# Kernel optimization log

Measured on AMD Instinct MI355X. Metric: run time of the kernel, lower is better.

## Reference

```python
import jax, jax.numpy as jnp
import numpy as np

N_HEAD = 16
N_KV_HEADS = 4
N_REP = 4
HEAD_DIM = 128
N_EMBD = 2048
EPS = 1e-5
ROPE_BASE = 10000.0


def setup_inputs() -> dict:
    key = jax.random.key(0)
    ks = jax.random.split(key, 5)
    B, T, C = 2, 2048, N_EMBD
    s = 0.02
    return {
        "x": jax.random.normal(ks[0], (B, T, C), dtype=jnp.float32),
        "wq": jax.random.normal(ks[1], (C, N_HEAD * HEAD_DIM), dtype=jnp.float32) * s,
        "wk": jax.random.normal(ks[2], (C, N_KV_HEADS * HEAD_DIM), dtype=jnp.float32) * s,
        "wv": jax.random.normal(ks[3], (C, N_KV_HEADS * HEAD_DIM), dtype=jnp.float32) * s,
        "wc": jax.random.normal(ks[4], (C, C), dtype=jnp.float32) * s,
        "q_norm_w": jnp.ones((HEAD_DIM,), dtype=jnp.float32),
        "k_norm_w": jnp.ones((HEAD_DIM,), dtype=jnp.float32),
    }


def _rmsnorm(x, w):
    # norm in fp32, scale by weight (matches RMSNorm.forward)
    xf = x.astype(jnp.float32)
    rms = jax.lax.rsqrt(jnp.mean(xf * xf, axis=-1, keepdims=True) + EPS)
    return (xf * rms).astype(x.dtype) * w


def _rope(x, cos, sin):
    # x: [B,T,H,D]; cos/sin: [T, D//2]; interleaved even/odd rotation
    xf = x.astype(jnp.float32)
    xe = xf[..., 0::2]
    xo = xf[..., 1::2]
    c = cos[None, :, None, :]
    s = sin[None, :, None, :]
    ye = xe * c - xo * s
    yo = xe * s + xo * c
    y = jnp.stack((ye, yo), axis=-1).reshape(x.shape)
    return y.astype(x.dtype)


def reference(x, wq, wk, wv, wc, q_norm_w, k_norm_w):
    B, T, C = x.shape
    q = (x @ wq).reshape(B, T, N_HEAD, HEAD_DIM)
    k = (x @ wk).reshape(B, T, N_KV_HEADS, HEAD_DIM)
    v = (x @ wv).reshape(B, T, N_KV_HEADS, HEAD_DIM)

    q = _rmsnorm(q, q_norm_w)
    k = _rmsnorm(k, k_norm_w)

    inv_freq = 1.0 / (ROPE_BASE ** (jnp.arange(0, HEAD_DIM, 2, dtype=jnp.float32) / HEAD_DIM))
    theta = jnp.arange(T, dtype=jnp.float32)[:, None] * inv_freq[None, :]  # [T, D//2]
    cos, sin = jnp.cos(theta), jnp.sin(theta)
    q = _rope(q, cos, sin)
    k = _rope(k, cos, sin)

    # GQA: repeat kv heads (repeat_kv with n_rep)
    k = jnp.repeat(k, N_REP, axis=2)  # [B,T,H,D]
    v = jnp.repeat(v, N_REP, axis=2)

    scale = 1.0 / jnp.sqrt(jnp.float32(HEAD_DIM))
    scores = jnp.einsum("bthd,bshd->bhts", q, k) * scale  # [B,H,T,S]
    causal = jnp.tril(jnp.ones((T, T), dtype=bool))
    scores = jnp.where(causal[None, None], scores, jnp.finfo(scores.dtype).min)
    attn = jax.nn.softmax(scores, axis=-1)
    y = jnp.einsum("bhts,bshd->bthd", attn, v).reshape(B, T, C)
    return y @ wc
```

## Files before the change

kernel.cpp:

```cpp
#include <hip/hip_runtime.h>
#include <hip/hip_bf16.h>
#include <cstdint>
#include <cstddef>

using bf16 = __hip_bfloat16;
typedef __attribute__((ext_vector_type(8))) short short8;
typedef __attribute__((ext_vector_type(4))) float f32x4;
typedef __attribute__((ext_vector_type(16))) float f32x16;

#define T_SEQ 2048
#define NHEAD 16
#define NKV 4
#define HD 128
#define CE 2048

__device__ __forceinline__ void gl_lds16(const void* g, void* l) {
  __builtin_amdgcn_global_load_lds(
      (const __attribute__((address_space(1))) unsigned int*)g,
      (__attribute__((address_space(3))) unsigned int*)l, 16, 0, 0);
}

__device__ __forceinline__ unsigned int cvtpk_bf16(float lo, float hi) {
  unsigned int r;
  asm("v_cvt_pk_bf16_f32 %0, %1, %2" : "=v"(r) : "v"(lo), "v"(hi));
  return r;
}

__device__ __forceinline__ void plswap(unsigned int& x, unsigned int& y, int hi) {
#if __has_builtin(__builtin_amdgcn_permlane32_swap)
  auto r = __builtin_amdgcn_permlane32_swap(x, y, false, false);
  x = r[0];
  y = r[1];
#else
  unsigned int xp = (unsigned int)__shfl_xor((int)x, 32);
  unsigned int yp = (unsigned int)__shfl_xor((int)y, 32);
  unsigned int nx = hi ? yp : x;
  unsigned int ny = hi ? y : xp;
  x = nx;
  y = ny;
#endif
}

__global__ void __launch_bounds__(256) prep(const float* __restrict__ x,
                                            const float* __restrict__ wq,
                                            const float* __restrict__ wk,
                                            const float* __restrict__ wv,
                                            const float* __restrict__ wc,
                                            bf16* __restrict__ xb,
                                            bf16* __restrict__ wqkvt,
                                            bf16* __restrict__ wct) {
  __shared__ float tile[32][33];
  const int tid = threadIdx.x;
  int bb = blockIdx.x;
  if (bb < 8192) {
    const int i = bb * 256 + tid;
    const float4 v = ((const float4*)x)[i];
    bf16 b0 = __float2bfloat16(v.x), b1 = __float2bfloat16(v.y),
         b2 = __float2bfloat16(v.z), b3 = __float2bfloat16(v.w);
    ushort4 u;
    u.x = *(const unsigned short*)&b0; u.y = *(const unsigned short*)&b1;
    u.z = *(const unsigned short*)&b2; u.w = *(const unsigned short*)&b3;
    ((ushort4*)xb)[i] = u;
    return;
  }
  bb -= 8192;
  const float* W;
  bf16* Wt;
  int N, bx, by;
  if (bb < 4096) {
    W = wq; Wt = wqkvt; N = 2048; bx = bb & 63; by = bb >> 6;
  } else if (bb < 5120) {
    const int c = bb - 4096;
    W = wk; Wt = wqkvt + (size_t)2048 * 2048; N = 512; bx = c & 15; by = c >> 4;
  } else if (bb < 6144) {
    const int c = bb - 5120;
    W = wv; Wt = wqkvt + (size_t)2560 * 2048; N = 512; bx = c & 15; by = c >> 4;
  } else {
    const int c = bb - 6144;
    W = wc; Wt = wct; N = 2048; bx = c & 63; by = c >> 6;
  }
  const int tx = tid & 31, ty = tid >> 5;
#pragma unroll
  for (int i = 0; i < 4; i++) {
    const int r = by * 32 + ty + i * 8;
    tile[ty + i * 8][tx] = W[(size_t)r * N + bx * 32 + tx];
  }
  __syncthreads();
#pragma unroll
  for (int i = 0; i < 4; i++) {
    const int n = bx * 32 + ty + i * 8;
    Wt[(size_t)n * 2048 + by * 32 + tx] = __float2bfloat16(tile[tx][ty + i * 8]);
  }
}

template <int BM, int BN, int WM, int WN, bool OBF>
__global__ void __launch_bounds__(512, 2)
gemm8i(const bf16* __restrict__ A, const bf16* __restrict__ Bt,
       void* __restrict__ Cv, int M, int N, int K) {
  constexpr int AWS = BM / 2 / WM;
  constexpr int BWS = BN / 2 / WN;
  constexpr int MH = AWS / 16;
  constexpr int NH = BWS / 16;
  constexpr int AH = BM / 128;
  constexpr int BH = BN / 128;
  constexpr int G = 2 * AH + BH;
  __shared__ bf16 smA[2][BM * 64];
  __shared__ bf16 smB[2][BN * 64];

  const int tid = threadIdx.x, lane = tid & 63, wid = tid >> 6;
  const int l15 = lane & 15, l4 = lane >> 4;
  const int wr = wid / WN, wc = wid % WN;

  const int nwg = gridDim.x;
  const int q = nwg >> 3, r = nwg & 7;
  const int xcd = blockIdx.x & 7, lin = blockIdx.x >> 3;
  const int wg = (xcd < r ? xcd * (q + 1) : r * (q + 1) + (xcd - r) * q) + lin;
  const int gw = N / BN;
  const int by = wg / gw, bx = wg % gw;
  const int row0 = by * BM, col0 = bx * BN;
  const int NT = K >> 6;
  const int NI = NT >> 1;

  const bf16* Ag = A + (size_t)row0 * K;
  const bf16* Bg = Bt + (size_t)col0 * K;

  auto stA = [&](int t, int h, int pb) {
    const int k0 = t << 6;
#pragma unroll
    for (int j = 0; j < AH; j++) {
      const int c = (h * AH + j) * 512 + tid;
      const int rowi = c >> 3;
      gl_lds16(Ag + (size_t)rowi * K + k0 + (((c & 7) ^ (rowi & 7)) << 3),
               (void*)(&smA[pb][(size_t)c << 3]));
    }
  };
  auto stB = [&](int t, int h, int pb) {
    const int k0 = t << 6;
#pragma unroll
    for (int j = 0; j < BH; j++) {
      const int c = (h * BH + j) * 512 + tid;
      const int rowi = c >> 3;
      gl_lds16(Bg + (size_t)rowi * K + k0 + (((c & 7) ^ (rowi & 7)) << 3),
               (void*)(&smB[pb][(size_t)c << 3]));
    }
  };
  auto rdA = [&](const bf16* sA, int mh, short8 (&dst)[MH][2]) {
#pragma unroll
    for (int i = 0; i < MH; i++) {
      const int rowl = mh * (BM / 2) + wr * AWS + i * 16 + l15;
#pragma unroll
      for (int kk = 0; kk < 2; kk++)
        dst[i][kk] = *(const short8*)(sA + rowl * 64 +
                                      ((((kk << 2) | l4) ^ (rowl & 7)) << 3));
    }
  };
  auto rdB = [&](const bf16* sB, int nh, short8 (&dst)[NH][2]) {
#pragma unroll
    for (int j = 0; j < NH; j++) {
      const int rowl = nh * (BN / 2) + wc * BWS + j * 16 + l15;
#pragma unroll
      for (int kk = 0; kk < 2; kk++)
        dst[j][kk] = *(const short8*)(sB + rowl * 64 +
                                      ((((kk << 2) | l4) ^ (rowl & 7)) << 3));
    }
  };

  f32x4 acc[2][2][MH][NH];
#pragma unroll
  for (int mh = 0; mh < 2; mh++)
#pragma unroll
    for (int nh = 0; nh < 2; nh++)
#pragma unroll
      for (int i = 0; i < MH; i++)
#pragma unroll
        for (int j = 0; j < NH; j++) acc[mh][nh][i][j] = (f32x4){0.f, 0.f, 0.f, 0.f};

  auto mmq = [&](short8 (&a)[MH][2], short8 (&b)[NH][2], f32x4 (&ac)[MH][NH]) {
    __builtin_amdgcn_s_setprio(1);
#pragma unroll
    for (int i = 0; i < MH; i++)
#pragma unroll
      for (int j = 0; j < NH; j++)
#pragma unroll
        for (int kk = 0; kk < 2; kk++)
          ac[i][j] = __builtin_amdgcn_mfma_f32_16x16x32_bf16(a[i][kk], b[j][kk],
                                                             ac[i][j], 0, 0, 0);
    __builtin_amdgcn_s_setprio(0);
  };

  short8 a0[MH][2], a1[MH][2], b0[NH][2], b1[NH][2];

#define LGKM0_SB                                            \
  asm volatile("s_waitcnt lgkmcnt(0)" ::: "memory");        \
  __builtin_amdgcn_sched_barrier(0);
#define GATE_G                                              \
  asm volatile("s_waitcnt vmcnt(%0)" ::"i"(G) : "memory");

  stA(0, 0, 0); stB(0, 0, 0); stA(0, 1, 0); stB(0, 1, 0);
  stA(1, 0, 1); stB(1, 0, 1); stA(1, 1, 1);
  GATE_G
  __builtin_amdgcn_s_barrier();

  for (int i = 0; i < NI - 1; ++i) {
    const int u = 2 * i, v = u + 1;
    stB(v, 1, 1);
    rdA(smA[0], 0, a0); rdB(smB[0], 0, b0);
    __builtin_amdgcn_s_barrier();
    LGKM0_SB
    mmq(a0, b0, acc[0][0]);
    __builtin_amdgcn_s_barrier();
    stA(u + 2, 0, 0);
    rdA(smA[0], 1, a1);
    __builtin_amdgcn_s_barrier();
    LGKM0_SB
    mmq(a1, b0, acc[1][0]);
    __builtin_amdgcn_s_barrier();
    stB(u + 2, 0, 0);
    rdB(smB[0], 1, b1);
    __builtin_amdgcn_s_barrier();
    LGKM0_SB
    mmq(a1, b1, acc[1][1]);
    __builtin_amdgcn_s_barrier();
    stA(u + 2, 1, 0);
    mmq(a0, b1, acc[0][1]);
    GATE_G
    __builtin_amdgcn_s_barrier();
    stB(u + 2, 1, 0);
    rdA(smA[1], 0, a0); rdB(smB[1], 0, b0);
    __builtin_amdgcn_s_barrier();
    LGKM0_SB
    mmq(a0, b0, acc[0][0]);
    __builtin_amdgcn_s_barrier();
    stA(v + 2, 0, 1);
    rdA(smA[1], 1, a1);
    __builtin_amdgcn_s_barrier();
    LGKM0_SB
    mmq(a1, b0, acc[1][0]);
    __builtin_amdgcn_s_barrier();
    stB(v + 2, 0, 1);
    rdB(smB[1], 1, b1);
    __builtin_amdgcn_s_barrier();
    LGKM0_SB
    mmq(a1, b1, acc[1][1]);
    __builtin_amdgcn_s_barrier();
    stA(v + 2, 1, 1);
    mmq(a0, b1, acc[0][1]);
    GATE_G
    __builtin_amdgcn_s_barrier();
  }

  {
    stB(NT - 1, 1, 1);
    rdA(smA[0], 0, a0); rdB(smB[0], 0, b0);
    __builtin_amdgcn_s_barrier();
    LGKM0_SB
    mmq(a0, b0, acc[0][0]);
    __builtin_amdgcn_s_barrier();
    rdA(smA[0], 1, a1);
    __builtin_amdgcn_s_barrier();
    LGKM0_SB
    mmq(a1, b0, acc[1][0]);
    __builtin_amdgcn_s_barrier();
    rdB(smB[0], 1, b1);
    __builtin_amdgcn_s_barrier();
    LGKM0_SB
    mmq(a1, b1, acc[1][1]);
    __builtin_amdgcn_s_barrier();
    mmq(a0, b1, acc[0][1]);
    asm volatile("s_waitcnt vmcnt(0)" ::: "memory");
    __builtin_amdgcn_s_barrier();
    rdA(smA[1], 0, a0); rdB(smB[1], 0, b0);
    __builtin_amdgcn_s_barrier();
    LGKM0_SB
    mmq(a0, b0, acc[0][0]);
    __builtin_amdgcn_s_barrier();
    rdA(smA[1], 1, a1);
    __builtin_amdgcn_s_barrier();
    LGKM0_SB
    mmq(a1, b0, acc[1][0]);
    __builtin_amdgcn_s_barrier();
    rdB(smB[1], 1, b1);
    __builtin_amdgcn_s_barrier();
    LGKM0_SB
    mmq(a1, b1, acc[1][1]);
    mmq(a0, b1, acc[0][1]);
  }

#pragma unroll
  for (int mh = 0; mh < 2; mh++)
#pragma unroll
    for (int nh = 0; nh < 2; nh++)
#pragma unroll
      for (int i = 0; i < MH; i++)
#pragma unroll
        for (int j = 0; j < NH; j++)
#pragma unroll
          for (int rr = 0; rr < 4; rr++) {
            const size_t row = row0 + mh * (BM / 2) + wr * AWS + i * 16 + l4 * 4 + rr;
            const size_t col = col0 + nh * (BN / 2) + wc * BWS + j * 16 + l15;
            if constexpr (OBF)
              ((bf16*)Cv)[row * N + col] = __float2bfloat16(acc[mh][nh][i][j][rr]);
            else
              ((float*)Cv)[row * N + col] = acc[mh][nh][i][j][rr];
          }
#undef LGKM0_SB
#undef GATE_G
}

__global__ void __launch_bounds__(256) qkv_post(const bf16* __restrict__ QKV,
                                                const float* __restrict__ qw,
                                                const float* __restrict__ kw,
                                                bf16* __restrict__ Qo,
                                                bf16* __restrict__ Ko,
                                                bf16* __restrict__ Vto) {
  const int g = blockIdx.x * 4 + (threadIdx.x >> 6);
  const int lane = threadIdx.x & 63;
  const int hh = g % 24;
  const int bt = g / 24;
  const int b = bt >> 11, t = bt & (T_SEQ - 1);
  int off;
  if (hh < 16) off = hh * 128;
  else if (hh < 20) off = 2048 + (hh - 16) * 128;
  else off = 2560 + (hh - 20) * 128;
  const ushort2 xr = *(const ushort2*)(QKV + (size_t)bt * 3072 + off + lane * 2);
  const float xx = __bfloat162float(*(const bf16*)&xr.x);
  const float xy = __bfloat162float(*(const bf16*)&xr.y);
  if (hh < 20) {
    float ss = xx * xx + xy * xy;
    ss += __shfl_xor(ss, 1);  ss += __shfl_xor(ss, 2);  ss += __shfl_xor(ss, 4);
    ss += __shfl_xor(ss, 8);  ss += __shfl_xor(ss, 16); ss += __shfl_xor(ss, 32);
    const float rms = rsqrtf(ss * (1.0f / 128.0f) + 1e-5f);
    const float* w = (hh < 16) ? qw : kw;
    const float x0 = xx * rms * w[lane * 2];
    const float x1 = xy * rms * w[lane * 2 + 1];
    const float inv = exp2f((float)lane * (-13.287712379549449f / 64.0f));
    const float th = (float)t * inv;
    const float sn = sinf(th), cs = cosf(th);
    const float y0 = x0 * cs - x1 * sn;
    const float y1 = x0 * sn + x1 * cs;
    const bf16 o0 = __float2bfloat16(y0), o1 = __float2bfloat16(y1);
    if (hh < 16) {
      bf16* d = Qo + ((size_t)(b * NHEAD + hh) * T_SEQ + t) * HD + lane * 2;
      d[0] = o0; d[1] = o1;
    } else {
      bf16* d = Ko + ((size_t)(b * NKV + (hh - 16)) * T_SEQ + t) * HD + lane * 2;
      d[0] = o0; d[1] = o1;
    }
  } else {
    bf16* d = Vto + ((size_t)(b * NKV + (hh - 20)) * HD + lane * 2) * T_SEQ + t;
    d[0] = __float2bfloat16(xx);
    d[T_SEQ] = __float2bfloat16(xy);
  }
}

__constant__ unsigned short JT[30] = {
    0x0605, 0x160A, 0x160B, 0x266B, 0x160F,
    0x0504, 0x1508, 0x1509, 0x2559, 0x256A, 0x150C, 0x150D, 0x255D,
    0x150E, 0x255E, 0x35AE, 0x256F, 0x35BF,
    0x0403, 0x1406, 0x1407, 0x2447, 0x2458, 0x245C, 0x349C, 0x34AD,
    0x0302, 0x2346,
    0x0201, 0x0100};

#define ATTN_CL 0.12754125f

__global__ void __launch_bounds__(256, 2) attn_fwd(const bf16* __restrict__ Q,
                                                   const bf16* __restrict__ K,
                                                   const bf16* __restrict__ Vt,
                                                   bf16* __restrict__ Y,
                                                   bf16* __restrict__ PO,
                                                   float* __restrict__ PML) {
  __shared__ bf16 smK[128 * 128];
  __shared__ bf16 smV[128 * 128];

  const int bid = blockIdx.x;
  const int bh = bid & 31;
  const int jobi = bid >> 5;
  const unsigned int e = JT[jobi];
  const int jq = e & 15;
  const int lo = (e >> 4) & 15;
  const int len = (e >> 8) & 15;
  const int part = e >> 12;
  const int hi_t = lo + len;

  const int h = bh & (NHEAD - 1), b = bh >> 4;
  const int bkv = b * NKV + (h >> 2);

  const int tid = threadIdx.x, wid = tid >> 6, lane = tid & 63;
  const int l31 = lane & 31, hi = lane >> 5;
  const int q0w = jq * 128 + wid * 32;
  const int trow = tid >> 4, tslot = tid & 15;

  const bf16* Kb = K + (size_t)bkv * T_SEQ * HD;
  const bf16* Vb = Vt + (size_t)bkv * HD * T_SEQ;

  const bf16* Qrow = Q + ((size_t)bh * T_SEQ + q0w + l31) * HD + hi * 8;
  short8 qf[8];
#pragma unroll
  for (int ds = 0; ds < 8; ds++) qf[ds] = *(const short8*)(Qrow + ds * 16);

  f32x16 o[4];
#pragma unroll
  for (int d = 0; d < 4; d++) o[d] = (f32x16)(0.f);
  float mrun = -INFINITY, lrun = 0.f;

  constexpr float CL = ATTN_CL;

  for (int t = lo; t < hi_t; t++) {
    const int k0 = t * 128;
    __syncthreads();
#pragma unroll
    for (int i = 0; i < 8; i++) {
      const int row = i * 16 + trow;
      const int ss = (tslot ^ (row & 15)) * 8;
      gl_lds16(Kb + (size_t)(k0 + row) * HD + ss, (void*)((char*)smK + i * 4096 + wid * 1024));
      gl_lds16(Vb + (size_t)row * T_SEQ + k0 + ss, (void*)((char*)smV + i * 4096 + wid * 1024));
    }
    __syncthreads();

    const bool diag = (t == jq);
    const int glim = diag ? wid : 3;

    f32x16 sg[4];
#pragma unroll
    for (int g = 0; g < 4; g++) {
      if (g > glim) continue;
      f32x16 acc = (f32x16)(0.f);
#pragma unroll
      for (int ds = 0; ds < 8; ds++) {
        const int row = g * 32 + l31;
        const short8 kf = *(const short8*)(smK + (size_t)row * 128 +
                                           (((ds << 1) | hi) ^ (row & 15)) * 8);
        acc = __builtin_amdgcn_mfma_f32_32x32x16_bf16(kf, qf[ds], acc, 0, 0, 0);
      }
      sg[g] = acc;
    }
    float tmax = -INFINITY;
#pragma unroll
    for (int g = 0; g < 4; g++) {
      if (g > glim) continue;
      if (diag && g == wid) {
#pragma unroll
        for (int r = 0; r < 16; r++) {
          const int kr = (r & 3) + 8 * (r >> 2) + (hi << 2);
          if (kr > l31) sg[g][r] = -INFINITY;
        }
      }
#pragma unroll
      for (int r = 0; r < 16; r++) tmax = fmaxf(tmax, sg[g][r]);
    }
    tmax = fmaxf(tmax, __shfl_xor(tmax, 32));
    const float mnew = fmaxf(mrun, tmax);
    const float f = exp2f((mrun - mnew) * CL);
    mrun = mnew;
    lrun *= f;
#pragma unroll
    for (int d = 0; d < 4; d++)
#pragma unroll
      for (int r = 0; r < 16; r++) o[d][r] *= f;

    float lsum = 0.f;
#pragma unroll
    for (int g = 0; g < 4; g++) {
      if (g > glim) continue;
      float pp[16];
      float s0 = 0.f, s1 = 0.f;
#pragma unroll
      for (int r = 0; r < 16; r++) pp[r] = exp2f((sg[g][r] - mnew) * CL);
#pragma unroll
      for (int r = 0; r < 8; r++) { s0 += pp[2 * r]; s1 += pp[2 * r + 1]; }
      lsum += s0 + s1;

      unsigned int w0 = cvtpk_bf16(pp[0], pp[1]),  w2 = cvtpk_bf16(pp[4], pp[5]);
      unsigned int w1 = cvtpk_bf16(pp[2], pp[3]),  w3 = cvtpk_bf16(pp[6], pp[7]);
      unsigned int w4 = cvtpk_bf16(pp[8], pp[9]),  w6 = cvtpk_bf16(pp[12], pp[13]);
      unsigned int w5 = cvtpk_bf16(pp[10], pp[11]), w7 = cvtpk_bf16(pp[14], pp[15]);
      plswap(w0, w2, hi); plswap(w1, w3, hi);
      plswap(w4, w6, hi); plswap(w5, w7, hi);
      union { unsigned int u[4]; short8 s8; } pa0, pa1;
      pa0.u[0] = w0; pa0.u[1] = w1; pa0.u[2] = w2; pa0.u[3] = w3;
      pa1.u[0] = w4; pa1.u[1] = w5; pa1.u[2] = w6; pa1.u[3] = w7;

#pragma unroll
      for (int d = 0; d < 4; d++) {
        const int row = d * 32 + l31;
        const int ks0 = g * 2, ks1 = g * 2 + 1;
        const short8 vf0 = *(const short8*)(smV + (size_t)row * 128 +
                                            (((ks0 << 1) | hi) ^ (row & 15)) * 8);
        const short8 vf1 = *(const short8*)(smV + (size_t)row * 128 +
                                            (((ks1 << 1) | hi) ^ (row & 15)) * 8);
        o[d] = __builtin_amdgcn_mfma_f32_32x32x16_bf16(vf0, pa0.s8, o[d], 0, 0, 0);
        o[d] = __builtin_amdgcn_mfma_f32_32x32x16_bf16(vf1, pa1.s8, o[d], 0, 0, 0);
      }
    }
    lrun += lsum + __shfl_xor(lsum, 32);
  }

  if (part == 0) {
    const float inv = 1.0f / lrun;
    bf16* yrow = Y + ((size_t)(b * T_SEQ + q0w + l31)) * CE + h * HD;
#pragma unroll
    for (int d = 0; d < 4; d++) {
#pragma unroll
      for (int rg = 0; rg < 4; rg++) {
        ushort4 u;
        bf16 e0 = __float2bfloat16(o[d][rg * 4 + 0] * inv);
        bf16 e1 = __float2bfloat16(o[d][rg * 4 + 1] * inv);
        bf16 e2 = __float2bfloat16(o[d][rg * 4 + 2] * inv);
        bf16 e3 = __float2bfloat16(o[d][rg * 4 + 3] * inv);
        u.x = *(const unsigned short*)&e0; u.y = *(const unsigned short*)&e1;
        u.z = *(const unsigned short*)&e2; u.w = *(const unsigned short*)&e3;
        *(ushort4*)(yrow + d * 32 + rg * 8 + (hi << 2)) = u;
      }
    }
  } else {
    const int plocal = (jq < 12) ? (jq - 6) * 2 + (part - 1)
                                 : 12 + (jq - 12) * 3 + (part - 1);
    const int pidx = bh * 24 + plocal;
    bf16* po = PO + (size_t)pidx * 16384;
    const int row = wid * 32 + l31;
#pragma unroll
    for (int d = 0; d < 4; d++) {
#pragma unroll
      for (int rg = 0; rg < 4; rg++) {
        ushort4 u;
        bf16 e0 = __float2bfloat16(o[d][rg * 4 + 0]);
        bf16 e1 = __float2bfloat16(o[d][rg * 4 + 1]);
        bf16 e2 = __float2bfloat16(o[d][rg * 4 + 2]);
        bf16 e3 = __float2bfloat16(o[d][rg * 4 + 3]);
        u.x = *(const unsigned short*)&e0; u.y = *(const unsigned short*)&e1;
        u.z = *(const unsigned short*)&e2; u.w = *(const unsigned short*)&e3;
        *(ushort4*)(po + (size_t)row * 128 + d * 32 + rg * 8 + (hi << 2)) = u;
      }
    }
    if (hi == 0) {
      PML[(size_t)pidx * 256 + row * 2 + 0] = mrun;
      PML[(size_t)pidx * 256 + row * 2 + 1] = lrun;
    }
  }
}

__global__ void __launch_bounds__(256) attn_combine(const bf16* __restrict__ PO,
                                                    const float* __restrict__ PML,
                                                    bf16* __restrict__ Y) {
  const int bid = blockIdx.x;
  const int rb = bid & 3;
  const int Jl = (bid >> 2) % 10;
  const int bh = bid / 40;
  const int J = 6 + Jl;
  const bool has2 = (J >= 12);
  const int base = bh * 24 + (has2 ? 12 + (J - 12) * 3 : (J - 6) * 2);
  const int tid = threadIdx.x;
  const int row = rb * 32 + (tid >> 3);
  const int c0 = (tid & 7) * 16;
  const int b = bh >> 4, h = bh & 15;

  const float m0 = PML[(size_t)(base + 0) * 256 + row * 2 + 0];
  const float l0 = PML[(size_t)(base + 0) * 256 + row * 2 + 1];
  const float m1 = PML[(size_t)(base + 1) * 256 + row * 2 + 0];
  const float l1 = PML[(size_t)(base + 1) * 256 + row * 2 + 1];
  float m2 = -INFINITY, l2 = 0.f;
  if (has2) {
    m2 = PML[(size_t)(base + 2) * 256 + row * 2 + 0];
    l2 = PML[(size_t)(base + 2) * 256 + row * 2 + 1];
  }
  const float mx = fmaxf(fmaxf(m0, m1), m2);
  const float w0 = exp2f((m0 - mx) * ATTN_CL);
  const float w1 = exp2f((m1 - mx) * ATTN_CL);
  const float w2 = has2 ? exp2f((m2 - mx) * ATTN_CL) : 0.f;
  const float inv = 1.0f / (w0 * l0 + w1 * l1 + w2 * l2);

  const bf16* p0 = PO + (size_t)(base + 0) * 16384 + (size_t)row * 128 + c0;
  const bf16* p1 = PO + (size_t)(base + 1) * 16384 + (size_t)row * 128 + c0;
  const bf16* p2 = PO + (size_t)(base + 2) * 16384 + (size_t)row * 128 + c0;

  float acc[16];
#pragma unroll
  for (int half = 0; half < 2; half++) {
    const short8 v0 = *(const short8*)(p0 + half * 8);
    const short8 v1 = *(const short8*)(p1 + half * 8);
#pragma unroll
    for (int i = 0; i < 8; i++) {
      const unsigned short u0 = (unsigned short)v0[i], u1 = (unsigned short)v1[i];
      acc[half * 8 + i] = w0 * __bfloat162float(*(const bf16*)&u0) +
                          w1 * __bfloat162float(*(const bf16*)&u1);
    }
  }
  if (has2) {
#pragma unroll
    for (int half = 0; half < 2; half++) {
      const short8 v2 = *(const short8*)(p2 + half * 8);
#pragma unroll
      for (int i = 0; i < 8; i++) {
        const unsigned short u2 = (unsigned short)v2[i];
        acc[half * 8 + i] += w2 * __bfloat162float(*(const bf16*)&u2);
      }
    }
  }

  bf16* yp = Y + ((size_t)(b * T_SEQ + J * 128 + row)) * CE + h * HD + c0;
#pragma unroll
  for (int half = 0; half < 2; half++) {
    short8 out;
#pragma unroll
    for (int i = 0; i < 8; i++) {
      const bf16 ev = __float2bfloat16(acc[half * 8 + i] * inv);
      out[i] = *(const short*)&ev;
    }
    *(short8*)(yp + half * 8) = out;
  }
}

extern "C" void kernel_launch(void* const* d_in, const int* in_sizes, int n_in,
                              void* d_out, int out_size, void* d_ws, size_t ws_size,
                              hipStream_t stream) {
  const float* x   = (const float*)d_in[0];
  const float* wq  = (const float*)d_in[1];
  const float* wk  = (const float*)d_in[2];
  const float* wv  = (const float*)d_in[3];
  const float* wc  = (const float*)d_in[4];
  const float* qnw = (const float*)d_in[5];
  const float* knw = (const float*)d_in[6];
  float* out = (float*)d_out;

  char* ws = (char*)d_ws;
  bf16*  xb    = (bf16*)(ws);
  bf16*  wqkvt = (bf16*)(ws + 16777216);
  bf16*  wct   = (bf16*)(ws + 29360128);
  bf16*  qkv   = (bf16*)(ws + 37748736);
  bf16*  partO = (bf16*)(ws + 37748736);
  float* partML= (float*)(ws + 62914560);
  bf16*  Qb    = (bf16*)(ws + 88080384);
  bf16*  Kb    = (bf16*)(ws + 104857600);
  bf16*  Vtb   = (bf16*)(ws + 109051904);
  bf16*  yb    = (bf16*)(ws + 113246208);

  prep<<<18432, 256, 0, stream>>>(x, wq, wk, wv, wc, xb, wqkvt, wct);
  gemm8i<256, 256, 2, 4, true><<<192, 512, 0, stream>>>(xb, wqkvt, qkv, 4096, 3072, 2048);
  qkv_post<<<24576, 256, 0, stream>>>(qkv, qnw, knw, Qb, Kb, Vtb);
  attn_fwd<<<960, 256, 0, stream>>>(Qb, Kb, Vtb, yb, partO, partML);
  attn_combine<<<1280, 256, 0, stream>>>(partO, partML, yb);
  gemm8i<128, 256, 2, 4, false><<<256, 512, 0, stream>>>(yb, wct, out, 4096, 2048, 2048);
}
```

Baseline: 218.0 us.

## Split-K the output projection GEMM with 256x256 tiles and a combine kernel

The output projection GEMM switches from 128x256 tiles to 256x256 tiles with K split in two, so the grid stays at 256 workgroups. Each half writes bf16 partials into workspace, and a new kernel sums them into the fp32 output. The aim is higher arithmetic intensity per tile while keeping all CUs busy. The cost is an extra launch, about 32MB of partial traffic, and an added bf16 rounding of the partials.

Measured after the change: 227.6 us. +4.4%, slower.

```diff
diff --git a/kernel.cpp b/kernel.cpp
--- a/kernel.cpp
+++ b/kernel.cpp
@@ -93,7 +93,7 @@
   }
 }
 
-template <int BM, int BN, int WM, int WN, bool OBF>
+template <int BM, int BN, int WM, int WN, bool OBF, bool KSPLIT = false>
 __global__ void __launch_bounds__(512, 2)
 gemm8i(const bf16* __restrict__ A, const bf16* __restrict__ Bt,
        void* __restrict__ Cv, int M, int N, int K) {
@@ -115,14 +115,19 @@
   const int q = nwg >> 3, r = nwg & 7;
   const int xcd = blockIdx.x & 7, lin = blockIdx.x >> 3;
   const int wg = (xcd < r ? xcd * (q + 1) : r * (q + 1) + (xcd - r) * q) + lin;
+  const int ntile = KSPLIT ? (nwg >> 1) : nwg;
+  const int kh = KSPLIT ? (wg / ntile) : 0;
+  const int tw = KSPLIT ? (wg % ntile) : wg;
   const int gw = N / BN;
-  const int by = wg / gw, bx = wg % gw;
+  const int by = tw / gw, bx = tw % gw;
   const int row0 = by * BM, col0 = bx * BN;
-  const int NT = K >> 6;
+  const int KT = KSPLIT ? (K >> 1) : K;
+  const int kbase = kh * KT;
+  const int NT = KT >> 6;
   const int NI = NT >> 1;
 
-  const bf16* Ag = A + (size_t)row0 * K;
-  const bf16* Bg = Bt + (size_t)col0 * K;
+  const bf16* Ag = A + (size_t)row0 * K + kbase;
+  const bf16* Bg = Bt + (size_t)col0 * K + kbase;
 
   auto stA = [&](int t, int h, int pb) {
     const int k0 = t << 6;
@@ -298,13 +303,31 @@
           for (int rr = 0; rr < 4; rr++) {
             const size_t row = row0 + mh * (BM / 2) + wr * AWS + i * 16 + l4 * 4 + rr;
             const size_t col = col0 + nh * (BN / 2) + wc * BWS + j * 16 + l15;
-            if constexpr (OBF)
+            if constexpr (KSPLIT)
+              ((bf16*)Cv)[(size_t)kh * M * N + row * N + col] =
+                  __float2bfloat16(acc[mh][nh][i][j][rr]);
+            else if constexpr (OBF)
               ((bf16*)Cv)[row * N + col] = __float2bfloat16(acc[mh][nh][i][j][rr]);
             else
               ((float*)Cv)[row * N + col] = acc[mh][nh][i][j][rr];
           }
 #undef LGKM0_SB
 #undef GATE_G
+}
+
+__global__ void __launch_bounds__(256) proj_combine(const bf16* __restrict__ P,
+                                                    float* __restrict__ out) {
+  const size_t i = ((size_t)blockIdx.x * 256 + threadIdx.x) * 8;
+  const short8 v0 = *(const short8*)(P + i);
+  const short8 v1 = *(const short8*)(P + 8388608 + i);
+  float o[8];
+#pragma unroll
+  for (int j = 0; j < 8; j++) {
+    const unsigned short u0 = (unsigned short)v0[j], u1 = (unsigned short)v1[j];
+    o[j] = __bfloat162float(*(const bf16*)&u0) + __bfloat162float(*(const bf16*)&u1);
+  }
+  *(float4*)(out + i) = (float4){o[0], o[1], o[2], o[3]};
+  *(float4*)(out + i + 4) = (float4){o[4], o[5], o[6], o[7]};
 }
 
 __global__ void __launch_bounds__(256) qkv_post(const bf16* __restrict__ QKV,
@@ -629,6 +652,7 @@
   bf16*  qkv   = (bf16*)(ws + 37748736);
   bf16*  partO = (bf16*)(ws + 37748736);
   float* partML= (float*)(ws + 62914560);
+  bf16*  projP = (bf16*)(ws + 37748736);
   bf16*  Qb    = (bf16*)(ws + 88080384);
   bf16*  Kb    = (bf16*)(ws + 104857600);
   bf16*  Vtb   = (bf16*)(ws + 109051904);
@@ -639,5 +663,6 @@
   qkv_post<<<24576, 256, 0, stream>>>(qkv, qnw, knw, Qb, Kb, Vtb);
   attn_fwd<<<960, 256, 0, stream>>>(Qb, Kb, Vtb, yb, partO, partML);
   attn_combine<<<1280, 256, 0, stream>>>(partO, partML, yb);
-  gemm8i<128, 256, 2, 4, false><<<256, 512, 0, stream>>>(yb, wct, out, 4096, 2048, 2048);
-}
+  gemm8i<256, 256, 2, 4, true, true><<<256, 512, 0, stream>>>(yb, wct, projP, 4096, 2048, 2048);
+  proj_combine<<<4096, 256, 0, stream>>>(projP, out);
+}
```

## Fuse QK RMSNorm, RoPE and V transpose into QKV GEMM epilogue

Applied to the files above, without the earlier changes.

Removes the separate qkv_post kernel and the intermediate bf16 QKV buffer. The QKV GEMM epilogue now does the per-head RMSNorm, with a cross-wave reduction through shared memory, then applies RoPE through lane shuffles and writes Q/K in head-major layout and V transposed. This saves a kernel launch plus a write and re-read of a 24MB intermediate. In exchange it adds sin/cos work and a shared-memory reduction to the GEMM tail, and the V transposed stores are strided and uncoalesced.

New measurement: 256.5 us. 17.6% more time.

```diff
diff --git a/kernel.cpp b/kernel.cpp
--- a/kernel.cpp
+++ b/kernel.cpp
@@ -93,10 +93,12 @@
   }
 }
 
-template <int BM, int BN, int WM, int WN, bool OBF>
+template <int BM, int BN, int WM, int WN, bool OBF, bool EPIQKV = false>
 __global__ void __launch_bounds__(512, 2)
 gemm8i(const bf16* __restrict__ A, const bf16* __restrict__ Bt,
-       void* __restrict__ Cv, int M, int N, int K) {
+       void* __restrict__ Cv, int M, int N, int K,
+       const float* __restrict__ qw, const float* __restrict__ kw,
+       bf16* __restrict__ Ko, bf16* __restrict__ Vto) {
   constexpr int AWS = BM / 2 / WM;
   constexpr int BWS = BN / 2 / WN;
   constexpr int MH = AWS / 16;
@@ -286,71 +288,106 @@
     mmq(a0, b1, acc[0][1]);
   }
 
-#pragma unroll
-  for (int mh = 0; mh < 2; mh++)
-#pragma unroll
-    for (int nh = 0; nh < 2; nh++)
-#pragma unroll
-      for (int i = 0; i < MH; i++)
-#pragma unroll
-        for (int j = 0; j < NH; j++)
+  if constexpr (EPIQKV) {
+    bf16* Qo = (bf16*)Cv;
+    float* red = (float*)&smA[0][0];
+    const int hbase = col0 >> 7;
+    const bool isV = (col0 >= 2560);
+    __builtin_amdgcn_s_barrier();
+    if (!isV) {
+#pragma unroll
+      for (int mh = 0; mh < 2; mh++)
+#pragma unroll
+        for (int nh = 0; nh < 2; nh++)
+#pragma unroll
+          for (int i = 0; i < MH; i++)
+#pragma unroll
+            for (int rr = 0; rr < 4; rr++) {
+              const float v0 = acc[mh][nh][i][0][rr];
+              const float v1 = acc[mh][nh][i][1][rr];
+              float s = v0 * v0 + v1 * v1;
+              s += __shfl_xor(s, 1); s += __shfl_xor(s, 2);
+              s += __shfl_xor(s, 4); s += __shfl_xor(s, 8);
+              if (l15 == i * 4 + rr)
+                red[((((wr * 2 + mh) * 2 + nh) * 64 + i * 16 + l4 * 4 + rr) << 2) + wc] = s;
+            }
+      __builtin_amdgcn_s_barrier();
+      const bool isK = (col0 >= 2048);
+      const float* wnorm = isK ? kw : qw;
+      const float wn0 = wnorm[wc * 32 + l15];
+      const float wn1 = wnorm[wc * 32 + 16 + l15];
+      const float invf0 = exp2f((float)((wc * 32 + l15) >> 1) * (-13.287712379549449f / 64.0f));
+      const float invf1 = exp2f((float)((wc * 32 + 16 + l15) >> 1) * (-13.287712379549449f / 64.0f));
+      const int odd = l15 & 1;
+#pragma unroll
+      for (int mh = 0; mh < 2; mh++)
+#pragma unroll
+        for (int i = 0; i < MH; i++)
 #pragma unroll
           for (int rr = 0; rr < 4; rr++) {
-            const size_t row = row0 + mh * (BM / 2) + wr * AWS + i * 16 + l4 * 4 + rr;
-            const size_t col = col0 + nh * (BN / 2) + wc * BWS + j * 16 + l15;
-            if constexpr (OBF)
-              ((bf16*)Cv)[row * N + col] = __float2bfloat16(acc[mh][nh][i][j][rr]);
-            else
-              ((float*)Cv)[row * N + col] = acc[mh][nh][i][j][rr];
+            const int row = row0 + mh * (BM / 2) + wr * AWS + i * 16 + l4 * 4 + rr;
+            const int tt = row & (T_SEQ - 1), bb2 = row >> 11;
+            const float s0 = sinf((float)tt * invf0), c0 = cosf((float)tt * invf0);
+            const float s1 = sinf((float)tt * invf1), c1 = cosf((float)tt * invf1);
+#pragma unroll
+            for (int nh = 0; nh < 2; nh++) {
+              const f32x4 p4 = *(const f32x4*)(red +
+                  ((((wr * 2 + mh) * 2 + nh) * 64 + i * 16 + l4 * 4 + rr) << 2));
+              const float rms = rsqrtf((p4[0] + p4[1] + p4[2] + p4[3]) * (1.0f / 128.0f) + 1e-5f);
+              const int hg = hbase + nh;
+              bf16* base = isK
+                  ? Ko + ((size_t)(bb2 * NKV + (hg - 16)) * T_SEQ + tt) * HD
+                  : Qo + ((size_t)(bb2 * NHEAD + hg) * T_SEQ + tt) * HD;
+#pragma unroll
+              for (int j = 0; j < 2; j++) {
+                const float v = acc[mh][nh][i][j][rr] * rms * (j ? wn1 : wn0);
+                const float p = __shfl_xor(v, 1);
+                const float cs = j ? c1 : c0, sn = j ? s1 : s0;
+                const float outv = odd ? (p * sn + v * cs) : (v * cs - p * sn);
+                base[wc * 32 + j * 16 + l15] = __float2bfloat16(outv);
+              }
+            }
           }
+    } else {
+#pragma unroll
+      for (int mh = 0; mh < 2; mh++)
+#pragma unroll
+        for (int nh = 0; nh < 2; nh++)
+#pragma unroll
+          for (int i = 0; i < MH; i++)
+#pragma unroll
+            for (int j = 0; j < 2; j++)
+#pragma unroll
+              for (int rr = 0; rr < 4; rr++) {
+                const int row = row0 + mh * (BM / 2) + wr * AWS + i * 16 + l4 * 4 + rr;
+                const int tt = row & (T_SEQ - 1), bb2 = row >> 11;
+                const int vh = hbase + nh - 20;
+                const int dd = wc * 32 + j * 16 + l15;
+                Vto[((size_t)(bb2 * NKV + vh) * HD + dd) * T_SEQ + tt] =
+                    __float2bfloat16(acc[mh][nh][i][j][rr]);
+              }
+    }
+  } else {
+#pragma unroll
+    for (int mh = 0; mh < 2; mh++)
+#pragma unroll
+      for (int nh = 0; nh < 2; nh++)
+#pragma unroll
+        for (int i = 0; i < MH; i++)
+#pragma unroll
+          for (int j = 0; j < NH; j++)
+#pragma unroll
+            for (int rr = 0; rr < 4; rr++) {
+              const size_t row = row0 + mh * (BM / 2) + wr * AWS + i * 16 + l4 * 4 + rr;
+              const size_t col = col0 + nh * (BN / 2) + wc * BWS + j * 16 + l15;
+              if constexpr (OBF)
+                ((bf16*)Cv)[row * N + col] = __float2bfloat16(acc[mh][nh][i][j][rr]);
+              else
+                ((float*)Cv)[row * N + col] = acc[mh][nh][i][j][rr];
+            }
+  }
 #undef LGKM0_SB
 #undef GATE_G
-}
-
-__global__ void __launch_bounds__(256) qkv_post(const bf16* __restrict__ QKV,
-                                                const float* __restrict__ qw,
-                                                const float* __restrict__ kw,
-                                                bf16* __restrict__ Qo,
-                                                bf16* __restrict__ Ko,
-                                                bf16* __restrict__ Vto) {
-  const int g = blockIdx.x * 4 + (threadIdx.x >> 6);
-  const int lane = threadIdx.x & 63;
-  const int hh = g % 24;
-  const int bt = g / 24;
-  const int b = bt >> 11, t = bt & (T_SEQ - 1);
-  int off;
-  if (hh < 16) off = hh * 128;
-  else if (hh < 20) off = 2048 + (hh - 16) * 128;
-  else off = 2560 + (hh - 20) * 128;
-  const ushort2 xr = *(const ushort2*)(QKV + (size_t)bt * 3072 + off + lane * 2);
-  const float xx = __bfloat162float(*(const bf16*)&xr.x);
-  const float xy = __bfloat162float(*(const bf16*)&xr.y);
-  if (hh < 20) {
-    float ss = xx * xx + xy * xy;
-    ss += __shfl_xor(ss, 1);  ss += __shfl_xor(ss, 2);  ss += __shfl_xor(ss, 4);
-    ss += __shfl_xor(ss, 8);  ss += __shfl_xor(ss, 16); ss += __shfl_xor(ss, 32);
-    const float rms = rsqrtf(ss * (1.0f / 128.0f) + 1e-5f);
-    const float* w = (hh < 16) ? qw : kw;
-    const float x0 = xx * rms * w[lane * 2];
-    const float x1 = xy * rms * w[lane * 2 + 1];
-    const float inv = exp2f((float)lane * (-13.287712379549449f / 64.0f));
-    const float th = (float)t * inv;
-    const float sn = sinf(th), cs = cosf(th);
-    const float y0 = x0 * cs - x1 * sn;
-    const float y1 = x0 * sn + x1 * cs;
-    const bf16 o0 = __float2bfloat16(y0), o1 = __float2bfloat16(y1);
-    if (hh < 16) {
-      bf16* d = Qo + ((size_t)(b * NHEAD + hh) * T_SEQ + t) * HD + lane * 2;
-      d[0] = o0; d[1] = o1;
-    } else {
-      bf16* d = Ko + ((size_t)(b * NKV + (hh - 16)) * T_SEQ + t) * HD + lane * 2;
-      d[0] = o0; d[1] = o1;
-    }
-  } else {
-    bf16* d = Vto + ((size_t)(b * NKV + (hh - 20)) * HD + lane * 2) * T_SEQ + t;
-    d[0] = __float2bfloat16(xx);
-    d[T_SEQ] = __float2bfloat16(xy);
-  }
 }
 
 __constant__ unsigned short JT[30] = {
@@ -626,7 +663,6 @@
   bf16*  xb    = (bf16*)(ws);
   bf16*  wqkvt = (bf16*)(ws + 16777216);
   bf16*  wct   = (bf16*)(ws + 29360128);
-  bf16*  qkv   = (bf16*)(ws + 37748736);
   bf16*  partO = (bf16*)(ws + 37748736);
   float* partML= (float*)(ws + 62914560);
   bf16*  Qb    = (bf16*)(ws + 88080384);
@@ -635,9 +671,10 @@
   bf16*  yb    = (bf16*)(ws + 113246208);
 
   prep<<<18432, 256, 0, stream>>>(x, wq, wk, wv, wc, xb, wqkvt, wct);
-  gemm8i<256, 256, 2, 4, true><<<192, 512, 0, stream>>>(xb, wqkvt, qkv, 4096, 3072, 2048);
-  qkv_post<<<24576, 256, 0, stream>>>(qkv, qnw, knw, Qb, Kb, Vtb);
+  gemm8i<256, 256, 2, 4, true, true><<<192, 512, 0, stream>>>(
+      xb, wqkvt, Qb, 4096, 3072, 2048, qnw, knw, Kb, Vtb);
   attn_fwd<<<960, 256, 0, stream>>>(Qb, Kb, Vtb, yb, partO, partML);
   attn_combine<<<1280, 256, 0, stream>>>(partO, partML, yb);
-  gemm8i<128, 256, 2, 4, false><<<256, 512, 0, stream>>>(yb, wct, out, 4096, 2048, 2048);
-}
+  gemm8i<128, 256, 2, 4, false, false><<<256, 512, 0, stream>>>(
+      yb, wct, out, 4096, 2048, 2048, nullptr, nullptr, nullptr, nullptr);
+}
```
